# Kernel tuning notes

Hardware: AMD Instinct MI355X
Metric: run time of the kernel (lower is better)

The kernel has to match this reference:

```python
import jax, jax.numpy as jnp
import numpy as np

# Architecture constants (match init_kwargs)
L, M, K, P, G = 3, 4096, 2, 4, 4
NUM_IN, NUM_OUT, B = 8192, 1000, 2048
F = 6          # number of combinact activation functions
EPS_BN = 1e-5  # BatchNorm1d eps
EPS = 1e-12    # numeric safety for sqrt


def setup_inputs() -> dict:
    key = jax.random.key(0)
    ks = jax.random.split(key, 8)
    x = jax.random.normal(ks[0], (B, NUM_IN), jnp.float32)
    # shuffle maps: perm 0 is identity (the un-permuted copy), perms 1..P-1 random
    rng = np.random.default_rng(0)
    perms = np.stack([
        np.stack([np.arange(M)] + [rng.permutation(M) for _ in range(P - 1)])
        for _ in range(L)
    ]).astype(np.int32)  # (L, P, M)
    cin_g = NUM_IN // G  # per-group input width (curr stays 8192 every layer)
    W = jax.random.normal(ks[1], (L, G, M // G, cin_g), jnp.float32) / np.sqrt(cin_g)
    b = jax.random.normal(ks[2], (L, G, M // G), jnp.float32) * 0.01
    gamma = jnp.ones((L, M), jnp.float32)
    beta = jnp.zeros((L, M), jnp.float32)
    # original inits alpha_primes to zeros; small random gives non-degenerate mixing
    alpha = jax.random.normal(ks[3], (L, P, F), jnp.float32) * 0.1
    d_last = (M // K) * P
    W_out = jax.random.normal(ks[4], (NUM_OUT, d_last), jnp.float32) / np.sqrt(d_last)
    b_out = jnp.zeros((NUM_OUT,), jnp.float32)
    return {"x": x, "perms": jnp.asarray(perms), "W": W, "b": b,
            "gamma": gamma, "beta": beta, "alpha": alpha,
            "W_out": W_out, "b_out": b_out}


def _combinact(z, alpha_l):
    # z: (B, clusters, K, P) -> (B, clusters, P); per-perm softmax mixing
    sig = jax.nn.sigmoid(z)
    pr = jnp.prod(z, axis=2)
    acts = jnp.stack([
        jnp.max(z, axis=2),                          # max
        jnp.sign(pr) * jnp.sqrt(jnp.abs(pr) + EPS),  # signed geomean (k=2)
        z[:, :, 0, :] * jnp.prod(sig, axis=2),       # swish-k
        jnp.sqrt(jnp.sum(z * z, axis=2) + EPS),      # l2
        jnp.max(jnp.abs(z), axis=2),                 # linf
        jax.nn.logsumexp(z, axis=2),                 # lse
    ], axis=0)  # (F, B, clusters, P)
    w = jax.nn.softmax(alpha_l, axis=-1)  # (P, F)
    return jnp.einsum('fbcp,pf->bcp', acts, w)


def _forward(x, perms, W, b, gamma, beta, alpha, W_out, b_out):
    h = x
    for l in range(L):
        C = h.shape[1]
        # grouped small linears: (B, C/G, G) x (G, M/G, C/G) -> (B, M/G, G) -> (B, M)
        hr = h.reshape(B, C // G, G)
        y = jnp.einsum('bcg,gmc->bmg', hr, W[l]) + b[l].T[None]
        y = y.reshape(B, M)
        # BatchNorm1d (training mode, biased batch var)
        mu = jnp.mean(y, axis=0)
        var = jnp.mean((y - mu) ** 2, axis=0)
        y = (y - mu) * jax.lax.rsqrt(var + EPS_BN) * gamma[l] + beta[l]
        # p permuted copies, reshape into clusters of k
        zc = y[:, perms[l]]                                   # (B, P, M) gather
        z = jnp.transpose(zc, (0, 2, 1)).reshape(B, M // K, K, P)
        a = _combinact(z, alpha[l])                           # (B, M/K, P)
        h = jnp.transpose(a, (0, 2, 1)).reshape(B, (M // K) * P)
    return h @ W_out.T + b_out


def reference(x, perms, W, b, gamma, beta, alpha, W_out, b_out):
    return _forward(x, perms, W, b, gamma, beta, alpha, W_out, b_out)
```

## Files before the change

kernel.cpp:

```cpp
#include <hip/hip_runtime.h>
#include <math.h>

#define Lnum 3
#define Mdim 4096
#define Pdim 4
#define Gdim 4
#define NIN 8192
#define NOUT 1000
#define Bdim 2048
#define Fdim 6
#define CIN 2048
#define MG 1024
#define CH 2048
#define DNEXT 8192
#define RCHUNK 128
#define NRCHUNK (Bdim / RCHUNK)

typedef short bf16x8 __attribute__((ext_vector_type(8)));
typedef float f32x4 __attribute__((ext_vector_type(4)));

__device__ __forceinline__ short f2bf(float f) {
    union { float f; unsigned u; } v; v.f = f;
    unsigned u = v.u;
    unsigned r = (u + 0x7fffu + ((u >> 16) & 1u)) >> 16;
    return (short)r;
}

__global__ __launch_bounds__(256) void convert_f32_bf16(
    const float* __restrict__ src, short* __restrict__ dst, int n8)
{
    int i = blockIdx.x * 256 + threadIdx.x;
    if (i >= n8) return;
    const float4* s = (const float4*)src + (size_t)i * 2;
    float4 v0 = s[0], v1 = s[1];
    bf16x8 o;
    o[0] = f2bf(v0.x); o[1] = f2bf(v0.y); o[2] = f2bf(v0.z); o[3] = f2bf(v0.w);
    o[4] = f2bf(v1.x); o[5] = f2bf(v1.y); o[6] = f2bf(v1.z); o[7] = f2bf(v1.w);
    *((bf16x8*)dst + i) = o;
}

__global__ __launch_bounds__(256) void convert_wo(
    const float* __restrict__ src, short* __restrict__ dst)
{
    int i = blockIdx.x * 256 + threadIdx.x;
    int row = i >> 10;
    bf16x8 o;
    if (row < NOUT) {
        const float4* s = (const float4*)(src + (size_t)row * DNEXT + (i & 1023) * 8);
        float4 v0 = s[0], v1 = s[1];
        o[0] = f2bf(v0.x); o[1] = f2bf(v0.y); o[2] = f2bf(v0.z); o[3] = f2bf(v0.w);
        o[4] = f2bf(v1.x); o[5] = f2bf(v1.y); o[6] = f2bf(v1.z); o[7] = f2bf(v1.w);
    } else {
        for (int j = 0; j < 8; ++j) o[j] = 0;
    }
    *((bf16x8*)dst + i) = o;
}

__global__ __launch_bounds__(256) void x_to_grouped(
    const float* __restrict__ x, short* __restrict__ hg)
{
    const int c = blockIdx.x * 256 + threadIdx.x;
    const int b = blockIdx.y;
    float4 v = *(const float4*)(x + (size_t)b * NIN + 4 * c);
    const size_t plane = (size_t)Bdim * CIN;
    hg[0 * plane + (size_t)b * CIN + c] = f2bf(v.x);
    hg[1 * plane + (size_t)b * CIN + c] = f2bf(v.y);
    hg[2 * plane + (size_t)b * CIN + c] = f2bf(v.z);
    hg[3 * plane + (size_t)b * CIN + c] = f2bf(v.w);
}

__global__ __launch_bounds__(256) void remap_perms(
    const int* __restrict__ perm, int* __restrict__ perm_g, int n)
{
    int i = blockIdx.x * 256 + threadIdx.x;
    if (i >= n) return;
    int j = perm[i];
    perm_g[i] = ((j & 3) << 10) | (j >> 2);
}

template<int BN_T, int NWARP>
__global__ __launch_bounds__(NWARP * 64) void gemm_mfma(
    const short* __restrict__ A0, size_t aZ, int lda,
    const short* __restrict__ B0, size_t bZ, int ldb,
    const float* __restrict__ bias0, size_t biasZ,
    float* __restrict__ C0, size_t cZ,
    int K, int ldc, int nbound)
{
    constexpr int NT   = NWARP * 64;
    constexpr int WCN  = NWARP / 2;
    constexpr int WCOL = BN_T / WCN;
    constexpr int FN   = WCOL / 16;

    const int nx = gridDim.x, ny = gridDim.y;
    const int nwg = nx * ny * gridDim.z;
    const int lin = blockIdx.x + nx * (blockIdx.y + ny * blockIdx.z);
    int swz = (lin & 7) * (nwg >> 3) + (lin >> 3);
    const int bx = swz % nx; swz /= nx;
    const int by = swz % ny;
    const int g  = swz / ny;

    const short* A  = A0 + aZ * g;
    const short* Bm = B0 + bZ * g;
    float* C = C0 + cZ * g;

    const int n0 = bx * BN_T;
    const int b0 = by * 128;

    __shared__ short As[2][128 * 64];
    __shared__ short Bs[2][BN_T * 64];

    const int tid  = threadIdx.x;
    const int w    = tid >> 6;
    const int lane = tid & 63;
    const int wr = w / WCN, wc = w % WCN;

    f32x4 acc[4][FN];
#pragma unroll
    for (int m = 0; m < 4; ++m)
#pragma unroll
        for (int n = 0; n < FN; ++n) acc[m][n] = (f32x4)0.f;

    auto stage = [&](int buf, int k0) {
#pragma unroll
        for (int idx = tid; idx < 128 * 8; idx += NT) {
            const int r = idx >> 3, slot = idx & 7;
            const int gs = slot ^ (r & 7);
            const short* ga = A + (size_t)(b0 + r) * lda + k0 + gs * 8;
            __builtin_amdgcn_global_load_lds(
                (const __attribute__((address_space(1))) void*)ga,
                (__attribute__((address_space(3))) void*)(&As[buf][idx * 8]), 16, 0, 0);
        }
#pragma unroll
        for (int idx = tid; idx < BN_T * 8; idx += NT) {
            const int r = idx >> 3, slot = idx & 7;
            const int gs = slot ^ (r & 7);
            const short* gb = Bm + (size_t)(n0 + r) * ldb + k0 + gs * 8;
            __builtin_amdgcn_global_load_lds(
                (const __attribute__((address_space(1))) void*)gb,
                (__attribute__((address_space(3))) void*)(&Bs[buf][idx * 8]), 16, 0, 0);
        }
    };

    const int fr15 = lane & 15;
    const int fq   = lane >> 4;

    auto compute = [&](int buf) {
#pragma unroll
        for (int kk = 0; kk < 2; ++kk) {
            bf16x8 af[4], bff[FN];
            const int kob = kk * 64 + fq * 16;
#pragma unroll
            for (int m = 0; m < 4; ++m) {
                const int r  = wr * 64 + m * 16 + fr15;
                const int sw = kob ^ ((r & 7) << 4);
                af[m] = *(const bf16x8*)(&As[buf][r * 64 + (sw >> 1)]);
            }
#pragma unroll
            for (int n = 0; n < FN; ++n) {
                const int r  = wc * WCOL + n * 16 + fr15;
                const int sw = kob ^ ((r & 7) << 4);
                bff[n] = *(const bf16x8*)(&Bs[buf][r * 64 + (sw >> 1)]);
            }
#pragma unroll
            for (int m = 0; m < 4; ++m)
#pragma unroll
                for (int n = 0; n < FN; ++n)
                    acc[m][n] = __builtin_amdgcn_mfma_f32_16x16x32_bf16(af[m], bff[n], acc[m][n], 0, 0, 0);
        }
    };

    stage(0, 0);
    asm volatile("s_waitcnt vmcnt(0)" ::: "memory");
    __builtin_amdgcn_s_barrier();
    asm volatile("" ::: "memory");

    const int nt = K >> 6;
    int cur = 0;
    for (int t = 0; t < nt; ++t) {
        if (t + 1 < nt) stage(cur ^ 1, (t + 1) << 6);
        compute(cur);
        asm volatile("s_waitcnt vmcnt(0)" ::: "memory");
        __builtin_amdgcn_s_barrier();
        asm volatile("" ::: "memory");
        cur ^= 1;
    }

#pragma unroll
    for (int m = 0; m < 4; ++m) {
#pragma unroll
        for (int n = 0; n < FN; ++n) {
#pragma unroll
            for (int j = 0; j < 4; ++j) {
                const int row = b0 + wr * 64 + m * 16 + fq * 4 + j;
                const int col = n0 + wc * WCOL + n * 16 + fr15;
                if (col < nbound) {
                    float v = acc[m][n][j];
                    if (bias0) v += bias0[biasZ * g + col];
                    C[(size_t)row * ldc + col] = v;
                }
            }
        }
    }
}

__global__ __launch_bounds__(256) void reduce_out(
    const float* __restrict__ part, const float* __restrict__ bo,
    float* __restrict__ out)
{
    const int n = blockIdx.x * 256 + threadIdx.x;
    const int b = blockIdx.y;
    if (n >= NOUT) return;
    const size_t S = (size_t)Bdim * 1024;
    const size_t i = (size_t)b * 1024 + n;
    out[(size_t)b * NOUT + n] =
        part[i] + part[S + i] + part[2 * S + i] + part[3 * S + i] + bo[n];
}

__global__ __launch_bounds__(256) void bn_stats(
    const float* __restrict__ Y, float* __restrict__ psum, float* __restrict__ psumsq)
{
    const int j  = blockIdx.x * 256 + threadIdx.x;
    const int r0 = blockIdx.y * RCHUNK;
    float s = 0.f, ss = 0.f;
    for (int r = 0; r < RCHUNK; ++r) {
        float v = Y[(size_t)(r0 + r) * Mdim + j];
        s += v; ss += v * v;
    }
    psum[blockIdx.y * Mdim + j]   = s;
    psumsq[blockIdx.y * Mdim + j] = ss;
}

__global__ __launch_bounds__(256) void bn_finalize(
    const float* __restrict__ psum, const float* __restrict__ psumsq,
    const float* __restrict__ gamma, const float* __restrict__ beta,
    float* __restrict__ scale, float* __restrict__ shift)
{
    const int jg = blockIdx.x * 256 + threadIdx.x;
    if (jg >= Mdim) return;
    const int j = ((jg & 1023) << 2) | (jg >> 10);
    float s = 0.f, ss = 0.f;
    for (int r = 0; r < NRCHUNK; ++r) {
        s  += psum[r * Mdim + jg];
        ss += psumsq[r * Mdim + jg];
    }
    const float mu  = s * (1.f / Bdim);
    const float var = ss * (1.f / Bdim) - mu * mu;
    const float sc  = gamma[j] * rsqrtf(var + 1e-5f);
    scale[jg] = sc;
    shift[jg] = beta[j] - mu * sc;
}

__global__ void alpha_softmax(const float* __restrict__ alpha, float* __restrict__ wsm)
{
    const int idx = threadIdx.x;
    if (idx >= Lnum * Pdim) return;
    const float* a = alpha + idx * Fdim;
    float mx = a[0];
#pragma unroll
    for (int f = 1; f < Fdim; ++f) mx = fmaxf(mx, a[f]);
    float e[Fdim]; float s = 0.f;
#pragma unroll
    for (int f = 0; f < Fdim; ++f) { e[f] = __expf(a[f] - mx); s += e[f]; }
    const float inv = 1.f / s;
#pragma unroll
    for (int f = 0; f < Fdim; ++f) wsm[idx * Fdim + f] = e[f] * inv;
}

template<int MODE>
__global__ __launch_bounds__(256) void combinact_kernel(
    const float* __restrict__ Y, const float* __restrict__ scale,
    const float* __restrict__ shift, const int* __restrict__ perm,
    const float* __restrict__ wsm, short* __restrict__ out)
{
    __shared__ float yn[Mdim];
    const int b   = blockIdx.x;
    const int tid = threadIdx.x;

#pragma unroll
    for (int k = 0; k < 4; ++k) {
        const int i4 = k * 256 + tid;
        const float4 v  = *(const float4*)(Y + (size_t)b * Mdim + (size_t)i4 * 4);
        const float4 sc = *(const float4*)(scale + i4 * 4);
        const float4 sh = *(const float4*)(shift + i4 * 4);
        float4 r;
        r.x = v.x * sc.x + sh.x;
        r.y = v.y * sc.y + sh.y;
        r.z = v.z * sc.z + sh.z;
        r.w = v.w * sc.w + sh.w;
        *(float4*)(yn + i4 * 4) = r;
    }
    __syncthreads();

    float wv[Pdim][Fdim];
#pragma unroll
    for (int p = 0; p < Pdim; ++p)
#pragma unroll
        for (int f = 0; f < Fdim; ++f) wv[p][f] = wsm[p * Fdim + f];

    const float L2E = 1.44269504f;
    const float LN2 = 0.69314718f;

#pragma unroll
    for (int k = 0; k < 8; ++k) {
        const int idx = k * 256 + tid;
        int c, g = 0, q = 0;
        if (MODE == 0) { g = idx >> 9; q = idx & 511; c = q * 4 + g; }
        else           { c = idx; }

#pragma unroll
        for (int p = 0; p < Pdim; ++p) {
            const int2 jj = *(const int2*)(perm + p * Mdim + 2 * c);
            const float z0 = yn[jj.x];
            const float z1 = yn[jj.y];

            const float mx = fmaxf(z0, z1);
            const float pr = z0 * z1;
            const float a1 = copysignf(__builtin_amdgcn_sqrtf(fabsf(pr) + 1e-12f), pr);

            const float e0 = __builtin_amdgcn_exp2f(-L2E * z0);
            const float e1 = __builtin_amdgcn_exp2f(-L2E * z1);
            const float a2 = z0 * __builtin_amdgcn_rcpf((1.f + e0) * (1.f + e1));

            const float a3 = __builtin_amdgcn_sqrtf(z0 * z0 + z1 * z1 + 1e-12f);
            const float a4 = fmaxf(fabsf(z0), fabsf(z1));

            const float ed = __builtin_amdgcn_exp2f(-L2E * fabsf(z0 - z1));
            const float a5 = mx + LN2 * __builtin_amdgcn_logf(1.f + ed);

            const float v = wv[p][0] * mx + wv[p][1] * a1 + wv[p][2] * a2 +
                            wv[p][3] * a3 + wv[p][4] * a4 + wv[p][5] * a5;

            if (MODE == 0)
                out[(size_t)g * ((size_t)Bdim * CIN) + (size_t)b * CIN + p * 512 + q] = f2bf(v);
            else
                out[(size_t)b * DNEXT + p * CH + c] = f2bf(v);
        }
    }
}

extern "C" void kernel_launch(void* const* d_in, const int* in_sizes, int n_in,
                              void* d_out, int out_size, void* d_ws, size_t ws_size,
                              hipStream_t stream)
{
    const float* x     = (const float*)d_in[0];
    const int*   perms = (const int*)  d_in[1];
    const float* W     = (const float*)d_in[2];
    const float* bvec  = (const float*)d_in[3];
    const float* gamma = (const float*)d_in[4];
    const float* beta  = (const float*)d_in[5];
    const float* alpha = (const float*)d_in[6];
    const float* Wo    = (const float*)d_in[7];
    const float* bo    = (const float*)d_in[8];
    float* out = (float*)d_out;

    char* ws = (char*)d_ws;
    float* y      = (float*)ws;
    short* hg     = (short*)(y + (size_t)Bdim * Mdim);
    short* hflat  = hg + (size_t)Gdim * Bdim * CIN;
    short* Wlb    = hflat + (size_t)Bdim * DNEXT;
    short* Wob    = Wlb + (size_t)Gdim * MG * CIN;
    float* psum   = (float*)(Wob + (size_t)1024 * DNEXT);
    float* psumsq = psum + (size_t)NRCHUNK * Mdim;
    float* scale  = psumsq + (size_t)NRCHUNK * Mdim;
    float* shift  = scale + Mdim;
    float* wsm    = shift + Mdim;
    int*   perm_g = (int*)(wsm + Lnum * Pdim * Fdim);

    float* part = (float*)hg;

    alpha_softmax<<<1, 64, 0, stream>>>(alpha, wsm);
    remap_perms<<<(Lnum * Pdim * Mdim) / 256, 256, 0, stream>>>(
        perms, perm_g, Lnum * Pdim * Mdim);
    convert_wo<<<(1024 * 1024) / 256, 256, 0, stream>>>(Wo, Wob);
    x_to_grouped<<<dim3(CIN / 256, Bdim), 256, 0, stream>>>(x, hg);

    const size_t planeA = (size_t)Bdim * CIN;
    const size_t planeB = (size_t)MG * CIN;

    for (int l = 0; l < Lnum; ++l) {
        convert_f32_bf16<<<(Gdim * MG * CIN / 8) / 256, 256, 0, stream>>>(
            W + (size_t)l * Gdim * MG * CIN, Wlb, Gdim * MG * CIN / 8);

        dim3 gg(MG / 128, Bdim / 128, Gdim);
        gemm_mfma<128, 8><<<gg, 512, 0, stream>>>(
            hg, planeA, CIN, Wlb, planeB, CIN,
            bvec + (size_t)l * Gdim * MG, (size_t)MG,
            y, (size_t)MG,
            CIN, Mdim, MG);

        dim3 gs(Mdim / 256, NRCHUNK);
        bn_stats<<<gs, 256, 0, stream>>>(y, psum, psumsq);
        bn_finalize<<<Mdim / 256, 256, 0, stream>>>(
            psum, psumsq, gamma + (size_t)l * Mdim, beta + (size_t)l * Mdim, scale, shift);

        if (l < Lnum - 1)
            combinact_kernel<0><<<Bdim, 256, 0, stream>>>(
                y, scale, shift, perm_g + (size_t)l * Pdim * Mdim, wsm + l * Pdim * Fdim, hg);
        else
            combinact_kernel<1><<<Bdim, 256, 0, stream>>>(
                y, scale, shift, perm_g + (size_t)l * Pdim * Mdim, wsm + l * Pdim * Fdim, hflat);
    }

    dim3 go(1024 / 128, Bdim / 128, 4);
    gemm_mfma<128, 8><<<go, 512, 0, stream>>>(
        hflat, (size_t)2048, DNEXT, Wob, (size_t)2048, DNEXT,
        nullptr, 0,
        part, (size_t)Bdim * 1024,
        2048, 1024, 1024);

    dim3 gr(4, Bdim);
    reduce_out<<<gr, 256, 0, stream>>>(part, bo, out);
}
```

Measured before the change: 351.6 us.

## Fuse BatchNorm statistics into GEMM epilogue and store activations in bf16

Each layer GEMM now accumulates per-column sum and sum-of-squares in its epilogue, reduces them across warps through shared memory, and writes per-row-tile partials. This replaces the separate bn_stats pass that re-read the fp32 output. The GEMM output is also stored as bf16, which halves the write and the later read in the combinact kernel. The cost is extra epilogue work and an LDS reduction, and the stats come from fp32 values while normalisation is applied to bf16-rounded values, a small precision mismatch.

After: 315.9 us. 10.1% less time.

```diff
diff --git a/kernel.cpp b/kernel.cpp
--- a/kernel.cpp
+++ b/kernel.cpp
@@ -13,8 +13,7 @@
 #define MG 1024
 #define CH 2048
 #define DNEXT 8192
-#define RCHUNK 128
-#define NRCHUNK (Bdim / RCHUNK)
+#define NRCHUNK (Bdim / 128)
 
 typedef short bf16x8 __attribute__((ext_vector_type(8)));
 typedef float f32x4 __attribute__((ext_vector_type(4)));
@@ -24,6 +23,11 @@
     unsigned u = v.u;
     unsigned r = (u + 0x7fffu + ((u >> 16) & 1u)) >> 16;
     return (short)r;
+}
+__device__ __forceinline__ float bf2f(short h) {
+    union { unsigned u; float f; } x;
+    x.u = ((unsigned)(unsigned short)h) << 16;
+    return x.f;
 }
 
 __global__ __launch_bounds__(256) void convert_f32_bf16(
@@ -78,13 +82,14 @@
     perm_g[i] = ((j & 3) << 10) | (j >> 2);
 }
 
-template<int BN_T, int NWARP>
+template<int BN_T, int NWARP, bool STATS, typename CT>
 __global__ __launch_bounds__(NWARP * 64) void gemm_mfma(
     const short* __restrict__ A0, size_t aZ, int lda,
     const short* __restrict__ B0, size_t bZ, int ldb,
     const float* __restrict__ bias0, size_t biasZ,
-    float* __restrict__ C0, size_t cZ,
-    int K, int ldc, int nbound)
+    CT* __restrict__ C0, size_t cZ,
+    int K, int ldc, int nbound,
+    float* __restrict__ psum, float* __restrict__ psumsq, int sgz)
 {
     constexpr int NT   = NWARP * 64;
     constexpr int WCN  = NWARP / 2;
@@ -101,7 +106,7 @@
 
     const short* A  = A0 + aZ * g;
     const short* Bm = B0 + bZ * g;
-    float* C = C0 + cZ * g;
+    CT* C = C0 + cZ * g;
 
     const int n0 = bx * BN_T;
     const int b0 = by * 128;
@@ -185,6 +190,10 @@
         cur ^= 1;
     }
 
+    float s[FN], ss[FN];
+#pragma unroll
+    for (int n = 0; n < FN; ++n) { s[n] = 0.f; ss[n] = 0.f; }
+
 #pragma unroll
     for (int m = 0; m < 4; ++m) {
 #pragma unroll
@@ -196,9 +205,34 @@
                 if (col < nbound) {
                     float v = acc[m][n][j];
                     if (bias0) v += bias0[biasZ * g + col];
-                    C[(size_t)row * ldc + col] = v;
+                    C[(size_t)row * ldc + col] = (CT)(sizeof(CT) == 2 ? (CT)f2bf(v) : (CT)v);
+                    if (STATS) { s[n] += v; ss[n] += v * v; }
                 }
             }
+        }
+    }
+
+    if (STATS) {
+        float* sum_lds = (float*)&As[0][0];
+        float* ssq_lds = sum_lds + BN_T * 8;
+        const int slot = wr * 4 + fq;
+#pragma unroll
+        for (int n = 0; n < FN; ++n) {
+            const int cl = wc * WCOL + n * 16 + fr15;
+            sum_lds[cl * 8 + slot] = s[n];
+            ssq_lds[cl * 8 + slot] = ss[n];
+        }
+        __syncthreads();
+        for (int cl = tid; cl < BN_T; cl += NT) {
+            float a = 0.f, b = 0.f;
+#pragma unroll
+            for (int q = 0; q < 8; ++q) {
+                a += sum_lds[cl * 8 + q];
+                b += ssq_lds[cl * 8 + q];
+            }
+            const size_t o = (size_t)by * Mdim + g * sgz + n0 + cl;
+            psum[o]   = a;
+            psumsq[o] = b;
         }
     }
 }
@@ -216,20 +250,6 @@
         part[i] + part[S + i] + part[2 * S + i] + part[3 * S + i] + bo[n];
 }
 
-__global__ __launch_bounds__(256) void bn_stats(
-    const float* __restrict__ Y, float* __restrict__ psum, float* __restrict__ psumsq)
-{
-    const int j  = blockIdx.x * 256 + threadIdx.x;
-    const int r0 = blockIdx.y * RCHUNK;
-    float s = 0.f, ss = 0.f;
-    for (int r = 0; r < RCHUNK; ++r) {
-        float v = Y[(size_t)(r0 + r) * Mdim + j];
-        s += v; ss += v * v;
-    }
-    psum[blockIdx.y * Mdim + j]   = s;
-    psumsq[blockIdx.y * Mdim + j] = ss;
-}
-
 __global__ __launch_bounds__(256) void bn_finalize(
     const float* __restrict__ psum, const float* __restrict__ psumsq,
     const float* __restrict__ gamma, const float* __restrict__ beta,
@@ -268,7 +288,7 @@
 
 template<int MODE>
 __global__ __launch_bounds__(256) void combinact_kernel(
-    const float* __restrict__ Y, const float* __restrict__ scale,
+    const short* __restrict__ Y, const float* __restrict__ scale,
     const float* __restrict__ shift, const int* __restrict__ perm,
     const float* __restrict__ wsm, short* __restrict__ out)
 {
@@ -277,17 +297,22 @@
     const int tid = threadIdx.x;
 
 #pragma unroll
-    for (int k = 0; k < 4; ++k) {
-        const int i4 = k * 256 + tid;
-        const float4 v  = *(const float4*)(Y + (size_t)b * Mdim + (size_t)i4 * 4);
-        const float4 sc = *(const float4*)(scale + i4 * 4);
-        const float4 sh = *(const float4*)(shift + i4 * 4);
-        float4 r;
-        r.x = v.x * sc.x + sh.x;
-        r.y = v.y * sc.y + sh.y;
-        r.z = v.z * sc.z + sh.z;
-        r.w = v.w * sc.w + sh.w;
-        *(float4*)(yn + i4 * 4) = r;
+    for (int k = 0; k < 2; ++k) {
+        const int i8 = k * 256 + tid;
+        bf16x8 v = *((const bf16x8*)(Y + (size_t)b * Mdim) + i8);
+        float4 sc0 = *(const float4*)(scale + i8 * 8);
+        float4 sc1 = *(const float4*)(scale + i8 * 8 + 4);
+        float4 sh0 = *(const float4*)(shift + i8 * 8);
+        float4 sh1 = *(const float4*)(shift + i8 * 8 + 4);
+        float* o = yn + i8 * 8;
+        o[0] = bf2f(v[0]) * sc0.x + sh0.x;
+        o[1] = bf2f(v[1]) * sc0.y + sh0.y;
+        o[2] = bf2f(v[2]) * sc0.z + sh0.z;
+        o[3] = bf2f(v[3]) * sc0.w + sh0.w;
+        o[4] = bf2f(v[4]) * sc1.x + sh1.x;
+        o[5] = bf2f(v[5]) * sc1.y + sh1.y;
+        o[6] = bf2f(v[6]) * sc1.z + sh1.z;
+        o[7] = bf2f(v[7]) * sc1.w + sh1.w;
     }
     __syncthreads();
 
@@ -354,8 +379,8 @@
     float* out = (float*)d_out;
 
     char* ws = (char*)d_ws;
-    float* y      = (float*)ws;
-    short* hg     = (short*)(y + (size_t)Bdim * Mdim);
+    short* y      = (short*)ws;
+    short* hg     = y + (size_t)Bdim * Mdim;
     short* hflat  = hg + (size_t)Gdim * Bdim * CIN;
     short* Wlb    = hflat + (size_t)Bdim * DNEXT;
     short* Wob    = Wlb + (size_t)Gdim * MG * CIN;
@@ -382,14 +407,13 @@
             W + (size_t)l * Gdim * MG * CIN, Wlb, Gdim * MG * CIN / 8);
 
         dim3 gg(MG / 128, Bdim / 128, Gdim);
-        gemm_mfma<128, 8><<<gg, 512, 0, stream>>>(
+        gemm_mfma<128, 8, true, short><<<gg, 512, 0, stream>>>(
             hg, planeA, CIN, Wlb, planeB, CIN,
             bvec + (size_t)l * Gdim * MG, (size_t)MG,
             y, (size_t)MG,
-            CIN, Mdim, MG);
-
-        dim3 gs(Mdim / 256, NRCHUNK);
-        bn_stats<<<gs, 256, 0, stream>>>(y, psum, psumsq);
+            CIN, Mdim, MG,
+            psum, psumsq, MG);
+
         bn_finalize<<<Mdim / 256, 256, 0, stream>>>(
             psum, psumsq, gamma + (size_t)l * Mdim, beta + (size_t)l * Mdim, scale, shift);
 
@@ -402,11 +426,12 @@
     }
 
     dim3 go(1024 / 128, Bdim / 128, 4);
-    gemm_mfma<128, 8><<<go, 512, 0, stream>>>(
+    gemm_mfma<128, 8, false, float><<<go, 512, 0, stream>>>(
         hflat, (size_t)2048, DNEXT, Wob, (size_t)2048, DNEXT,
         nullptr, 0,
         part, (size_t)Bdim * 1024,
-        2048, 1024, 1024);
+        2048, 1024, 1024,
+        nullptr, nullptr, 0);
 
     dim3 gr(4, Bdim);
     reduce_out<<<gr, 256, 0, stream>>>(part, bo, out);
```
